# Kernel tuning notes

Hardware: AMD Instinct MI355X
Metric: run time of the kernel (lower is better)

The kernel has to match this reference:

```python
import jax, jax.numpy as jnp
import numpy as np

NUM_EXPERTS = 64
TOP_K = 2

def setup_inputs() -> dict:
    key = jax.random.key(0)
    k1, k2, k3, k4 = jax.random.split(key, 4)
    B, N, C, E = 4, 4096, 2048, NUM_EXPERTS
    x = jax.random.normal(k1, (B, N, C), dtype=jnp.float32)
    routing_context = jax.random.normal(k2, (B, C), dtype=jnp.float32)
    # Linear(C, E, bias=False) and Linear(C, C, bias=False), torch layout (out, in)
    gate_w = jax.random.normal(k3, (E, C), dtype=jnp.float32) * (1.0 / np.sqrt(C))
    ctx_w = jax.random.normal(k4, (C, C), dtype=jnp.float32) * (1.0 / np.sqrt(C))
    return {"x": x, "routing_context": routing_context, "gate_w": gate_w, "ctx_w": ctx_w}

def reference(x, routing_context, gate_w, ctx_w):
    B, N, C = x.shape
    T = B * N
    E = gate_w.shape[0]
    # context_proj(routing_context): (B,C) @ (C,C)^T -> broadcast over N
    ctx = routing_context @ ctx_w.T                      # (B, C)
    x_routing = (x + ctx[:, None, :]).reshape(T, C)      # (T, C)
    logits = x_routing @ gate_w.T                        # (T, E)
    top_vals, top_idx = jax.lax.top_k(logits, TOP_K)     # (T, K) each
    top_weights = jax.nn.softmax(top_vals, axis=-1)      # (T, K)
    probs = jax.nn.softmax(logits, axis=-1)              # (T, E)
    importance = probs.sum(axis=0) / T                   # (E,)
    # load: fraction of tokens that pick each expert in their top-k
    load = jnp.zeros((E,), dtype=probs.dtype).at[top_idx.reshape(-1)].add(1.0) / T
    aux_loss = E * (importance * load).sum()
    return top_idx, top_weights, aux_loss
```

## Files before the change

kernel.cpp:

```cpp
#include <hip/hip_runtime.h>
#include <math.h>

#define T_TOKENS 16384
#define C_DIM    2048
#define N_SEQ    4096
#define E_EXP    64
#define KC       32
#define TM       64
#define LSTR     36
#define NSLICE   4
#define EPB      1024

__global__ __launch_bounds__(256) void ctx_kernel(
    const float* __restrict__ rc, const float* __restrict__ ctx_w,
    float* __restrict__ ctx_out)
{
    const int w    = threadIdx.x >> 6;
    const int lane = threadIdx.x & 63;
    const int o    = blockIdx.x * 4 + w;
    const int b    = o >> 11;
    const int j    = o & 2047;

    const float4* wr = (const float4*)(ctx_w + (size_t)j * C_DIM);
    const float4* rr = (const float4*)(rc + (size_t)b * C_DIM);
    float s = 0.f;
#pragma unroll
    for (int it = 0; it < 8; ++it) {
        float4 a = wr[it * 64 + lane];
        float4 c = rr[it * 64 + lane];
        s += a.x * c.x + a.y * c.y + a.z * c.z + a.w * c.w;
    }
#pragma unroll
    for (int off = 32; off; off >>= 1) s += __shfl_xor(s, off, 64);
    if (lane == 0) ctx_out[b * C_DIM + j] = s;
}

__global__ __launch_bounds__(256) void gemm_kernel(
    const float* __restrict__ x, const float* __restrict__ gate_w,
    const float* __restrict__ ctx, float* __restrict__ P)
{
    __shared__ float xs[TM][LSTR];
    __shared__ float gs[E_EXP][LSTR];

    const int tid   = threadIdx.x;
    const int eg    = tid & 15;
    const int tg    = tid >> 4;
    const int tile  = blockIdx.x & 255;
    const int slice = blockIdx.x >> 8;
    const int t0    = tile * TM;
    const int b     = t0 / N_SEQ;
    const int cbase = slice * (C_DIM / NSLICE);

    const int scg = tid & 7;
    const int sr  = tid >> 3;

    const float* ctx_row = ctx + (size_t)b * C_DIM;

    float4 acc[4][4];
#pragma unroll
    for (int i = 0; i < 4; ++i)
#pragma unroll
        for (int j = 0; j < 4; ++j)
            acc[i][j] = make_float4(0.f, 0.f, 0.f, 0.f);

    float4 px[2], pg[2], pc;
    auto prefetch = [&](int kc) {
        const int c0 = cbase + kc * KC + scg * 4;
        pc    = *(const float4*)(ctx_row + c0);
        px[0] = *(const float4*)(x + (size_t)(t0 + sr) * C_DIM + c0);
        px[1] = *(const float4*)(x + (size_t)(t0 + sr + 32) * C_DIM + c0);
        pg[0] = *(const float4*)(gate_w + (size_t)sr * C_DIM + c0);
        pg[1] = *(const float4*)(gate_w + (size_t)(sr + 32) * C_DIM + c0);
    };

    prefetch(0);
    const int NCHUNK = (C_DIM / NSLICE) / KC;
    for (int kc = 0; kc < NCHUNK; ++kc) {
        __syncthreads();
        {
            float4 v0 = px[0], v1 = px[1];
            v0.x += pc.x; v0.y += pc.y; v0.z += pc.z; v0.w += pc.w;
            v1.x += pc.x; v1.y += pc.y; v1.z += pc.z; v1.w += pc.w;
            *(float4*)&xs[sr][scg * 4]      = v0;
            *(float4*)&xs[sr + 32][scg * 4] = v1;
            *(float4*)&gs[sr][scg * 4]      = pg[0];
            *(float4*)&gs[sr + 32][scg * 4] = pg[1];
        }
        __syncthreads();
        if (kc + 1 < NCHUNK) prefetch(kc + 1);
#pragma unroll
        for (int cc = 0; cc < KC; cc += 4) {
            float4 xv[4], gv[4];
#pragma unroll
            for (int i = 0; i < 4; ++i) xv[i] = *(const float4*)&xs[tg + 16 * i][cc];
#pragma unroll
            for (int j = 0; j < 4; ++j) gv[j] = *(const float4*)&gs[eg + 16 * j][cc];
#pragma unroll
            for (int i = 0; i < 4; ++i)
#pragma unroll
                for (int j = 0; j < 4; ++j) {
                    acc[i][j].x = fmaf(xv[i].x, gv[j].x, acc[i][j].x);
                    acc[i][j].y = fmaf(xv[i].y, gv[j].y, acc[i][j].y);
                    acc[i][j].z = fmaf(xv[i].z, gv[j].z, acc[i][j].z);
                    acc[i][j].w = fmaf(xv[i].w, gv[j].w, acc[i][j].w);
                }
        }
    }

    float* Ps = P + (size_t)slice * T_TOKENS * E_EXP;
#pragma unroll
    for (int i = 0; i < 4; ++i)
#pragma unroll
        for (int j = 0; j < 4; ++j)
            Ps[(size_t)(t0 + tg + 16 * i) * E_EXP + eg + 16 * j] =
                (acc[i][j].x + acc[i][j].y) + (acc[i][j].z + acc[i][j].w);
}

__global__ __launch_bounds__(256) void epilogue_kernel(
    const float* __restrict__ P, float* __restrict__ out,
    float* __restrict__ bp)
{
    __shared__ float red[4][128];

    const int tid  = threadIdx.x;
    const int wv   = tid >> 6;
    const int lane = tid & 63;
    const int t0   = blockIdx.x * (T_TOKENS / EPB);

    float imp_acc = 0.f, cnt_acc = 0.f;

    for (int tt = 0; tt < 4; ++tt) {
        const int t = t0 + wv * 4 + tt;
        float v = 0.f;
#pragma unroll
        for (int s = 0; s < NSLICE; ++s)
            v += P[((size_t)s * T_TOKENS + t) * E_EXP + lane];

        const float p = expf(v);
        float v1 = v;  int i1 = lane;
        float v2 = -INFINITY; int i2 = 0x7fffffff;
        float s = p;
#pragma unroll
        for (int off = 32; off; off >>= 1) {
            float ov1 = __shfl_xor(v1, off, 64);
            int   oi1 = __shfl_xor(i1, off, 64);
            float ov2 = __shfl_xor(v2, off, 64);
            int   oi2 = __shfl_xor(i2, off, 64);
            s += __shfl_xor(s, off, 64);
            const bool aw = (ov1 < v1) || (ov1 == v1 && i1 < oi1);
            const float lv = aw ? ov1 : v1;  const int li = aw ? oi1 : i1;
            const float wv2 = aw ? v2 : ov2; const int wi = aw ? i2 : oi2;
            if (!aw) { v1 = ov1; i1 = oi1; }
            const bool sw = (wv2 < lv) || (wv2 == lv && li < wi);
            v2 = sw ? lv : wv2; i2 = sw ? li : wi;
        }

        imp_acc += p / s;
        if (lane == i1 || lane == i2) cnt_acc += 1.f;

        if (lane == 0) {
            const float e2 = expf(v2 - v1);
            const float w1 = 1.f / (1.f + e2);
            const float w2 = e2 / (1.f + e2);
            out[2 * t]     = (float)i1;
            out[2 * t + 1] = (float)i2;
            out[2 * T_TOKENS + 2 * t]     = w1;
            out[2 * T_TOKENS + 2 * t + 1] = w2;
        }
    }

    red[wv][lane]      = imp_acc;
    red[wv][64 + lane] = cnt_acc;
    __syncthreads();
    if (tid < 128) {
        float s = red[0][tid] + red[1][tid] + red[2][tid] + red[3][tid];
        bp[(size_t)blockIdx.x * 128 + tid] = s;
    }
}

__global__ __launch_bounds__(1024) void aux_kernel(
    const float* __restrict__ bp, int nb, float* __restrict__ out_aux)
{
    __shared__ float4 red[32][32];
    const int tid = threadIdx.x;
    const int c4  = tid & 31;
    const int grp = tid >> 5;

    const float4* bp4 = (const float4*)bp;
    float4 s = make_float4(0.f, 0.f, 0.f, 0.f);
    for (int r = grp; r < nb; r += 32) {
        float4 v = bp4[(size_t)r * 32 + c4];
        s.x += v.x; s.y += v.y; s.z += v.z; s.w += v.w;
    }
    red[grp][c4] = s;
    __syncthreads();

    if (tid < 32) {
        float4 t = make_float4(0.f, 0.f, 0.f, 0.f);
#pragma unroll
        for (int g = 0; g < 32; ++g) {
            float4 v = red[g][tid];
            t.x += v.x; t.y += v.y; t.z += v.z; t.w += v.w;
        }
        red[0][tid] = t;
    }
    __syncthreads();

    if (tid < 16) {
        float4 a = red[0][tid];
        float4 b = red[0][tid + 16];
        float v = a.x * b.x + a.y * b.y + a.z * b.z + a.w * b.w;
#pragma unroll
        for (int off = 8; off; off >>= 1) v += __shfl_xor(v, off, 64);
        if (tid == 0)
            out_aux[0] = (float)E_EXP * v / ((float)T_TOKENS * (float)T_TOKENS);
    }
}

#define FKC   64
#define FLSTR 68
__global__ __launch_bounds__(256) void router_fused_kernel(
    const float* __restrict__ x, const float* __restrict__ gate_w,
    const float* __restrict__ ctx, float* __restrict__ out,
    float* __restrict__ bp)
{
    __shared__ float xs[TM][FLSTR];
    __shared__ float gs[E_EXP][FLSTR];
    __shared__ float ls[TM][FLSTR];
    __shared__ float red[4][128];

    const int tid = threadIdx.x;
    const int eg  = tid & 15;
    const int tg  = tid >> 4;
    const int t0  = blockIdx.x * TM;
    const int b   = t0 / N_SEQ;
    const int sr  = tid >> 4;
    const int scg = tid & 15;
    const float* ctx_row = ctx + (size_t)b * C_DIM;

    float4 acc[4][4];
#pragma unroll
    for (int i = 0; i < 4; ++i)
#pragma unroll
        for (int j = 0; j < 4; ++j) acc[i][j] = make_float4(0.f, 0.f, 0.f, 0.f);

    float4 px[4], pg[4], pc;
    auto prefetch = [&](int kc) {
        const int c0 = kc * FKC + scg * 4;
        pc = *(const float4*)(ctx_row + c0);
#pragma unroll
        for (int i = 0; i < 4; ++i) {
            px[i] = *(const float4*)(x + (size_t)(t0 + sr + 16 * i) * C_DIM + c0);
            pg[i] = *(const float4*)(gate_w + (size_t)(sr + 16 * i) * C_DIM + c0);
        }
    };

    prefetch(0);
    const int NCHUNK = C_DIM / FKC;
    for (int kc = 0; kc < NCHUNK; ++kc) {
        __syncthreads();
#pragma unroll
        for (int i = 0; i < 4; ++i) {
            float4 v = px[i];
            v.x += pc.x; v.y += pc.y; v.z += pc.z; v.w += pc.w;
            *(float4*)&xs[sr + 16 * i][scg * 4] = v;
            *(float4*)&gs[sr + 16 * i][scg * 4] = pg[i];
        }
        __syncthreads();
        if (kc + 1 < NCHUNK) prefetch(kc + 1);
#pragma unroll
        for (int cc = 0; cc < FKC; cc += 4) {
            float4 xv[4], gv[4];
#pragma unroll
            for (int i = 0; i < 4; ++i) xv[i] = *(const float4*)&xs[tg + 16 * i][cc];
#pragma unroll
            for (int j = 0; j < 4; ++j) gv[j] = *(const float4*)&gs[eg + 16 * j][cc];
#pragma unroll
            for (int i = 0; i < 4; ++i)
#pragma unroll
                for (int j = 0; j < 4; ++j) {
                    acc[i][j].x = fmaf(xv[i].x, gv[j].x, acc[i][j].x);
                    acc[i][j].y = fmaf(xv[i].y, gv[j].y, acc[i][j].y);
                    acc[i][j].z = fmaf(xv[i].z, gv[j].z, acc[i][j].z);
                    acc[i][j].w = fmaf(xv[i].w, gv[j].w, acc[i][j].w);
                }
        }
    }

    __syncthreads();
#pragma unroll
    for (int i = 0; i < 4; ++i)
#pragma unroll
        for (int j = 0; j < 4; ++j)
            ls[tg + 16 * i][eg + 16 * j] =
                (acc[i][j].x + acc[i][j].y) + (acc[i][j].z + acc[i][j].w);
    __syncthreads();

    const int wv   = tid >> 6;
    const int lane = tid & 63;
    float imp_acc = 0.f, cnt_acc = 0.f;

    for (int tt = 0; tt < 16; ++tt) {
        const int tokL = wv * 16 + tt;
        const float v = ls[tokL][lane];
        const float p = expf(v);
        float v1 = v;  int i1 = lane;
        float v2 = -INFINITY; int i2 = 0x7fffffff;
        float s = p;
#pragma unroll
        for (int off = 32; off; off >>= 1) {
            float ov1 = __shfl_xor(v1, off, 64);
            int   oi1 = __shfl_xor(i1, off, 64);
            float ov2 = __shfl_xor(v2, off, 64);
            int   oi2 = __shfl_xor(i2, off, 64);
            s += __shfl_xor(s, off, 64);
            const bool aw = (ov1 < v1) || (ov1 == v1 && i1 < oi1);
            const float lv = aw ? ov1 : v1;  const int li = aw ? oi1 : i1;
            const float wv2 = aw ? v2 : ov2; const int wi = aw ? i2 : oi2;
            if (!aw) { v1 = ov1; i1 = oi1; }
            const bool sw = (wv2 < lv) || (wv2 == lv && li < wi);
            v2 = sw ? lv : wv2; i2 = sw ? li : wi;
        }
        imp_acc += p / s;
        if (lane == i1 || lane == i2) cnt_acc += 1.f;
        if (lane == 0) {
            const int t = t0 + tokL;
            const float e2 = expf(v2 - v1);
            const float w1 = 1.f / (1.f + e2);
            const float w2 = e2 / (1.f + e2);
            out[2 * t]     = (float)i1;
            out[2 * t + 1] = (float)i2;
            out[2 * T_TOKENS + 2 * t]     = w1;
            out[2 * T_TOKENS + 2 * t + 1] = w2;
        }
    }

    red[wv][lane]      = imp_acc;
    red[wv][64 + lane] = cnt_acc;
    __syncthreads();
    if (tid < 128) {
        float s = red[0][tid] + red[1][tid] + red[2][tid] + red[3][tid];
        bp[(size_t)blockIdx.x * 128 + tid] = s;
    }
}

extern "C" void kernel_launch(void* const* d_in, const int* in_sizes, int n_in,
                              void* d_out, int out_size, void* d_ws, size_t ws_size,
                              hipStream_t stream)
{
    (void)in_sizes; (void)n_in; (void)out_size;
    const float* x      = (const float*)d_in[0];
    const float* rc     = (const float*)d_in[1];
    const float* gate_w = (const float*)d_in[2];
    const float* ctx_w  = (const float*)d_in[3];
    float* out = (float*)d_out;

    float* ctx = (float*)d_ws;
    float* P   = ctx + 8192;
    float* bp  = P + (size_t)NSLICE * T_TOKENS * E_EXP;

    const size_t need =
        (8192 + (size_t)NSLICE * T_TOKENS * E_EXP + (size_t)EPB * 128) * sizeof(float);

    ctx_kernel<<<2048, 256, 0, stream>>>(rc, ctx_w, ctx);
    if (ws_size >= need) {
        gemm_kernel<<<256 * NSLICE, 256, 0, stream>>>(x, gate_w, ctx, P);
        epilogue_kernel<<<EPB, 256, 0, stream>>>(P, out, bp);
        aux_kernel<<<1, 1024, 0, stream>>>(bp, EPB, out + 2 * 2 * T_TOKENS);
    } else {
        float* bpf = ctx + 8192;
        router_fused_kernel<<<256, 256, 0, stream>>>(x, gate_w, ctx, out, bpf);
        aux_kernel<<<1, 1024, 0, stream>>>(bpf, 256, out + 2 * 2 * T_TOKENS);
    }
}
```

Before: 272.5 us.

## Compute gating GEMM with bf16x3 split MFMA instead of FP32 FMA

Replaces the scalar FP32 FMA gating GEMM with matrix-core MFMA bf16 instructions. Each FP32 operand is split into three bf16 parts and six cross products are accumulated to keep accuracy close to FP32. A new pre-pass splits gate_w into a fragment-friendly bf16 layout in workspace, and x is split on the fly into shared memory. This trades conversion ALU work and six MFMAs per tile for relief from the FP32 FMA bottleneck. The kernel still has to read all of x, which is large.

```diff
diff --git a/kernel.cpp b/kernel.cpp
--- a/kernel.cpp
+++ b/kernel.cpp
@@ -5,11 +5,45 @@
 #define C_DIM    2048
 #define N_SEQ    4096
 #define E_EXP    64
-#define KC       32
+#define NSLICE   4
+#define KSLICE   512
+#define KC       64
 #define TM       64
-#define LSTR     36
-#define NSLICE   4
 #define EPB      1024
+#define XSTR     72
+#define GN       131072
+
+typedef __attribute__((ext_vector_type(8))) short  short8;
+typedef __attribute__((ext_vector_type(4))) float  floatx4;
+
+__device__ __forceinline__ void split3(float v, ushort& h, ushort& m, ushort& l) {
+    unsigned u = __float_as_uint(v);
+    unsigned r = (u + 0x7fffu + ((u >> 16) & 1u)) >> 16;
+    h = (ushort)r;
+    float e1 = v - __uint_as_float(r << 16);
+    u = __float_as_uint(e1);
+    r = (u + 0x7fffu + ((u >> 16) & 1u)) >> 16;
+    m = (ushort)r;
+    float e2 = e1 - __uint_as_float(r << 16);
+    u = __float_as_uint(e2);
+    r = (u + 0x7fffu + ((u >> 16) & 1u)) >> 16;
+    l = (ushort)r;
+}
+
+__global__ __launch_bounds__(256) void gsplit_kernel(
+    const float* __restrict__ gw, ushort* __restrict__ gsp)
+{
+    const int idx  = blockIdx.x * 256 + threadIdx.x;
+    const int j    = idx & 7;
+    const int e    = (idx >> 3) & 63;
+    const int koct = idx >> 9;
+    float g = gw[(size_t)e * C_DIM + koct * 8 + j];
+    ushort h, m, l;
+    split3(g, h, m, l);
+    gsp[idx]          = h;
+    gsp[GN + idx]     = m;
+    gsp[2 * GN + idx] = l;
+}
 
 __global__ __launch_bounds__(256) void ctx_kernel(
     const float* __restrict__ rc, const float* __restrict__ ctx_w,
@@ -35,85 +69,98 @@
     if (lane == 0) ctx_out[b * C_DIM + j] = s;
 }
 
-__global__ __launch_bounds__(256) void gemm_kernel(
-    const float* __restrict__ x, const float* __restrict__ gate_w,
+__global__ __launch_bounds__(256) void gemm_mfma_kernel(
+    const float* __restrict__ x, const ushort* __restrict__ gsp,
     const float* __restrict__ ctx, float* __restrict__ P)
 {
-    __shared__ float xs[TM][LSTR];
-    __shared__ float gs[E_EXP][LSTR];
+    __shared__ ushort xs[3][TM][XSTR];
 
     const int tid   = threadIdx.x;
-    const int eg    = tid & 15;
-    const int tg    = tid >> 4;
     const int tile  = blockIdx.x & 255;
     const int slice = blockIdx.x >> 8;
     const int t0    = tile * TM;
     const int b     = t0 / N_SEQ;
-    const int cbase = slice * (C_DIM / NSLICE);
-
-    const int scg = tid & 7;
-    const int sr  = tid >> 3;
+    const int cbase = slice * KSLICE;
+
+    const int w    = tid >> 6;
+    const int lane = tid & 63;
+    const int l15  = lane & 15;
+    const int quad = lane >> 4;
+
+    const int sr = tid >> 2;
+    const int sq = tid & 3;
 
     const float* ctx_row = ctx + (size_t)b * C_DIM;
 
-    float4 acc[4][4];
-#pragma unroll
-    for (int i = 0; i < 4; ++i)
-#pragma unroll
-        for (int j = 0; j < 4; ++j)
-            acc[i][j] = make_float4(0.f, 0.f, 0.f, 0.f);
-
-    float4 px[2], pg[2], pc;
+    floatx4 acc[4];
+#pragma unroll
+    for (int nt = 0; nt < 4; ++nt) acc[nt] = (floatx4){0.f, 0.f, 0.f, 0.f};
+
+    float4 px[4];
     auto prefetch = [&](int kc) {
-        const int c0 = cbase + kc * KC + scg * 4;
-        pc    = *(const float4*)(ctx_row + c0);
-        px[0] = *(const float4*)(x + (size_t)(t0 + sr) * C_DIM + c0);
-        px[1] = *(const float4*)(x + (size_t)(t0 + sr + 32) * C_DIM + c0);
-        pg[0] = *(const float4*)(gate_w + (size_t)sr * C_DIM + c0);
-        pg[1] = *(const float4*)(gate_w + (size_t)(sr + 32) * C_DIM + c0);
+        const float4* xr =
+            (const float4*)(x + (size_t)(t0 + sr) * C_DIM + cbase + kc * KC);
+#pragma unroll
+        for (int i = 0; i < 4; ++i) px[i] = xr[sq + 4 * i];
     };
 
     prefetch(0);
-    const int NCHUNK = (C_DIM / NSLICE) / KC;
+    const int NCHUNK = KSLICE / KC;
     for (int kc = 0; kc < NCHUNK; ++kc) {
         __syncthreads();
         {
-            float4 v0 = px[0], v1 = px[1];
-            v0.x += pc.x; v0.y += pc.y; v0.z += pc.z; v0.w += pc.w;
-            v1.x += pc.x; v1.y += pc.y; v1.z += pc.z; v1.w += pc.w;
-            *(float4*)&xs[sr][scg * 4]      = v0;
-            *(float4*)&xs[sr + 32][scg * 4] = v1;
-            *(float4*)&gs[sr][scg * 4]      = pg[0];
-            *(float4*)&gs[sr + 32][scg * 4] = pg[1];
+            const float4* cr =
+                (const float4*)(ctx_row + cbase + kc * KC);
+#pragma unroll
+            for (int i = 0; i < 4; ++i) {
+                float4 c = cr[sq + 4 * i];
+                float4 v = px[i];
+                v.x += c.x; v.y += c.y; v.z += c.z; v.w += c.w;
+                ushort4 h, m, l;
+                split3(v.x, h.x, m.x, l.x);
+                split3(v.y, h.y, m.y, l.y);
+                split3(v.z, h.z, m.z, l.z);
+                split3(v.w, h.w, m.w, l.w);
+                const int col = (sq + 4 * i) * 4;
+                *(ushort4*)&xs[0][sr][col] = h;
+                *(ushort4*)&xs[1][sr][col] = m;
+                *(ushort4*)&xs[2][sr][col] = l;
+            }
         }
         __syncthreads();
         if (kc + 1 < NCHUNK) prefetch(kc + 1);
-#pragma unroll
-        for (int cc = 0; cc < KC; cc += 4) {
-            float4 xv[4], gv[4];
-#pragma unroll
-            for (int i = 0; i < 4; ++i) xv[i] = *(const float4*)&xs[tg + 16 * i][cc];
-#pragma unroll
-            for (int j = 0; j < 4; ++j) gv[j] = *(const float4*)&gs[eg + 16 * j][cc];
-#pragma unroll
-            for (int i = 0; i < 4; ++i)
-#pragma unroll
-                for (int j = 0; j < 4; ++j) {
-                    acc[i][j].x = fmaf(xv[i].x, gv[j].x, acc[i][j].x);
-                    acc[i][j].y = fmaf(xv[i].y, gv[j].y, acc[i][j].y);
-                    acc[i][j].z = fmaf(xv[i].z, gv[j].z, acc[i][j].z);
-                    acc[i][j].w = fmaf(xv[i].w, gv[j].w, acc[i][j].w);
-                }
-        }
-    }
-
-    float* Ps = P + (size_t)slice * T_TOKENS * E_EXP;
-#pragma unroll
-    for (int i = 0; i < 4; ++i)
-#pragma unroll
-        for (int j = 0; j < 4; ++j)
-            Ps[(size_t)(t0 + tg + 16 * i) * E_EXP + eg + 16 * j] =
-                (acc[i][j].x + acc[i][j].y) + (acc[i][j].z + acc[i][j].w);
+
+#pragma unroll
+        for (int s = 0; s < 2; ++s) {
+            const int colk = s * 32 + quad * 8;
+            short8 ah = *(const short8*)&xs[0][16 * w + l15][colk];
+            short8 am = *(const short8*)&xs[1][16 * w + l15][colk];
+            short8 al = *(const short8*)&xs[2][16 * w + l15][colk];
+
+            const int koct0 = (cbase + kc * KC + s * 32) >> 3;
+            const int fib   = (koct0 + quad) * 64 + l15;
+#pragma unroll
+            for (int nt = 0; nt < 4; ++nt) {
+                const size_t fo = (size_t)(fib + 16 * nt) * 8;
+                short8 bh = *(const short8*)(gsp + fo);
+                short8 bm = *(const short8*)(gsp + GN + fo);
+                short8 bl = *(const short8*)(gsp + 2 * (size_t)GN + fo);
+                acc[nt] = __builtin_amdgcn_mfma_f32_16x16x32_bf16(ah, bh, acc[nt], 0, 0, 0);
+                acc[nt] = __builtin_amdgcn_mfma_f32_16x16x32_bf16(ah, bm, acc[nt], 0, 0, 0);
+                acc[nt] = __builtin_amdgcn_mfma_f32_16x16x32_bf16(am, bh, acc[nt], 0, 0, 0);
+                acc[nt] = __builtin_amdgcn_mfma_f32_16x16x32_bf16(ah, bl, acc[nt], 0, 0, 0);
+                acc[nt] = __builtin_amdgcn_mfma_f32_16x16x32_bf16(al, bh, acc[nt], 0, 0, 0);
+                acc[nt] = __builtin_amdgcn_mfma_f32_16x16x32_bf16(am, bm, acc[nt], 0, 0, 0);
+            }
+        }
+    }
+
+    float* Ps = P + ((size_t)slice * T_TOKENS + t0 + 16 * w) * E_EXP;
+#pragma unroll
+    for (int nt = 0; nt < 4; ++nt)
+#pragma unroll
+        for (int r = 0; r < 4; ++r)
+            Ps[(size_t)(quad * 4 + r) * E_EXP + 16 * nt + l15] = acc[nt][r];
 }
 
 __global__ __launch_bounds__(256) void epilogue_kernel(
@@ -160,12 +207,10 @@
 
         if (lane == 0) {
             const float e2 = expf(v2 - v1);
-            const float w1 = 1.f / (1.f + e2);
-            const float w2 = e2 / (1.f + e2);
             out[2 * t]     = (float)i1;
             out[2 * t + 1] = (float)i2;
-            out[2 * T_TOKENS + 2 * t]     = w1;
-            out[2 * T_TOKENS + 2 * t + 1] = w2;
+            out[2 * T_TOKENS + 2 * t]     = 1.f / (1.f + e2);
+            out[2 * T_TOKENS + 2 * t + 1] = e2 / (1.f + e2);
         }
     }
 
@@ -326,12 +371,10 @@
         if (lane == 0) {
             const int t = t0 + tokL;
             const float e2 = expf(v2 - v1);
-            const float w1 = 1.f / (1.f + e2);
-            const float w2 = e2 / (1.f + e2);
             out[2 * t]     = (float)i1;
             out[2 * t + 1] = (float)i2;
-            out[2 * T_TOKENS + 2 * t]     = w1;
-            out[2 * T_TOKENS + 2 * t + 1] = w2;
+            out[2 * T_TOKENS + 2 * t]     = 1.f / (1.f + e2);
+            out[2 * T_TOKENS + 2 * t + 1] = e2 / (1.f + e2);
         }
     }
 
@@ -355,21 +398,23 @@
     const float* ctx_w  = (const float*)d_in[3];
     float* out = (float*)d_out;
 
-    float* ctx = (float*)d_ws;
-    float* P   = ctx + 8192;
-    float* bp  = P + (size_t)NSLICE * T_TOKENS * E_EXP;
+    float*  ctx = (float*)d_ws;
+    float*  bp  = ctx + 8192;
+    float*  P   = bp + (size_t)EPB * 128;
+    ushort* gsp = (ushort*)(P + (size_t)NSLICE * T_TOKENS * E_EXP);
 
     const size_t need =
-        (8192 + (size_t)NSLICE * T_TOKENS * E_EXP + (size_t)EPB * 128) * sizeof(float);
+        (8192 + (size_t)EPB * 128 + (size_t)NSLICE * T_TOKENS * E_EXP) * sizeof(float)
+        + (size_t)3 * GN * sizeof(ushort);
 
     ctx_kernel<<<2048, 256, 0, stream>>>(rc, ctx_w, ctx);
     if (ws_size >= need) {
-        gemm_kernel<<<256 * NSLICE, 256, 0, stream>>>(x, gate_w, ctx, P);
+        gsplit_kernel<<<GN / 256, 256, 0, stream>>>(gate_w, gsp);
+        gemm_mfma_kernel<<<256 * NSLICE, 256, 0, stream>>>(x, gsp, ctx, P);
         epilogue_kernel<<<EPB, 256, 0, stream>>>(P, out, bp);
         aux_kernel<<<1, 1024, 0, stream>>>(bp, EPB, out + 2 * 2 * T_TOKENS);
     } else {
-        float* bpf = ctx + 8192;
-        router_fused_kernel<<<256, 256, 0, stream>>>(x, gate_w, ctx, out, bpf);
-        aux_kernel<<<1, 1024, 0, stream>>>(bpf, 256, out + 2 * 2 * T_TOKENS);
-    }
-}
+        router_fused_kernel<<<256, 256, 0, stream>>>(x, gate_w, ctx, out, bp);
+        aux_kernel<<<1, 1024, 0, stream>>>(bp, 256, out + 2 * 2 * T_TOKENS);
+    }
+}
```

Measured after the change: 258.6 us. 1.05x faster.
